# Optimization experiments

Measured on AMD Instinct MI355X. Metric: run time of the kernel, lower is better.

Reference implementation:

```python
import jax, jax.numpy as jnp
import numpy as np

DIM = 768
NUM_HEADS = 12
HEAD_DIM = DIM // NUM_HEADS
SCALE = HEAD_DIM ** -0.5


def setup_inputs() -> dict:
    key = jax.random.key(0)
    k1, k2, k3, k4 = jax.random.split(key, 4)
    x = jax.random.normal(k1, (8, 1024, DIM), dtype=jnp.float32)
    # torch Linear weights are [out, in]; no qkv bias (qkv_bias=False)
    qkv_w = jax.random.normal(k2, (3 * DIM, DIM), dtype=jnp.float32) * (DIM ** -0.5)
    proj_w = jax.random.normal(k3, (DIM, DIM), dtype=jnp.float32) * (DIM ** -0.5)
    proj_b = jax.random.normal(k4, (DIM,), dtype=jnp.float32) * 0.02
    return {"x": x, "qkv_w": qkv_w, "proj_w": proj_w, "proj_b": proj_b}


def reference(x, qkv_w, proj_w, proj_b):
    B, N, C = x.shape
    # qkv: [B, N, 3C] -> [3, B, H, N, D]
    qkv = jnp.einsum('bnc,oc->bno', x, qkv_w)
    qkv = qkv.reshape(B, N, 3, NUM_HEADS, HEAD_DIM).transpose(2, 0, 3, 1, 4)
    q, k, v = qkv[0], qkv[1], qkv[2]
    attn = jnp.einsum('bhnd,bhmd->bhnm', q, k) * SCALE
    attn = jax.nn.softmax(attn, axis=-1)
    out = jnp.einsum('bhnm,bhmd->bhnd', attn, v)  # [B, H, N, D]
    out = out.transpose(0, 2, 1, 3).reshape(B, N, C)
    out = jnp.einsum('bnc,oc->bno', out, proj_w) + proj_b
    return out
```

## Files before the change

### kernel.cpp

```cpp
#include <hip/hip_runtime.h>

typedef short bf16x8 __attribute__((ext_vector_type(8)));
typedef float f32x4 __attribute__((ext_vector_type(4)));
typedef float f32x16 __attribute__((ext_vector_type(16)));

#define AS1 __attribute__((address_space(1)))
#define AS3 __attribute__((address_space(3)))

__device__ __forceinline__ void gload16(const void* g, void* l) {
  __builtin_amdgcn_global_load_lds((const AS1 void*)g, (AS3 void*)l, 16, 0, 0);
}

__device__ __forceinline__ unsigned short f2bf(float f) {
  union { float f; unsigned u; } v; v.f = f;
  unsigned r = v.u + 0x7FFFu + ((v.u >> 16) & 1u);
  return (unsigned short)(r >> 16);
}

__device__ __forceinline__ unsigned cvtpk(float a, float b) {
  unsigned r;
  asm("v_cvt_pk_bf16_f32 %0, %1, %2" : "=v"(r) : "v"(a), "v"(b));
  return r;
}
__device__ __forceinline__ void plswap(unsigned& d, unsigned& s) {
  asm("v_permlane32_swap_b32 %0, %1" : "+v"(d), "+v"(s));
}


__global__ __launch_bounds__(256) void cast_all(
    const float* __restrict__ x, const float* __restrict__ w1, const float* __restrict__ w2,
    unsigned short* __restrict__ xb, unsigned short* __restrict__ w1b,
    unsigned short* __restrict__ w2b) {
  int i = blockIdx.x * blockDim.x + threadIdx.x;
  const float* in; unsigned short* out;
  if (i < 1572864) { in = x; out = xb; }
  else if (i < 2015232) { i -= 1572864; in = w1; out = w1b; }
  else { i -= 2015232; in = w2; out = w2b; }
  float4 v = reinterpret_cast<const float4*>(in)[i];
  ushort4 o; o.x = f2bf(v.x); o.y = f2bf(v.y); o.z = f2bf(v.z); o.w = f2bf(v.w);
  reinterpret_cast<ushort4*>(out)[i] = o;
}

template<int MODE>
__global__ __launch_bounds__(256) void gemm128(
    const unsigned short* __restrict__ A, const unsigned short* __restrict__ B,
    int K, int N,
    unsigned short* __restrict__ Qh, unsigned short* __restrict__ Kh,
    unsigned short* __restrict__ Vt,
    float* __restrict__ Cf, const float* __restrict__ bias) {
  constexpr int BM = (MODE == 0) ? 128 : 64;
  constexpr int MREP = BM / 32;
  constexpr int NX = (MODE == 0) ? 18 : 6;
  constexpr int CPX = (MODE == 0) ? 144 : 96;
  __shared__ unsigned short Ab[BM * 64];
  __shared__ unsigned short Bb[128 * 64];
  const int tid = threadIdx.x, lane = tid & 63, wave = tid >> 6;
  const int l15 = lane & 15, lhi = lane >> 4;
  const int bid = blockIdx.x;
  const int s = (bid & 7) * CPX + (bid >> 3);
  const int m0 = (s / NX) * BM, n0 = (s % NX) * 128;
  const int wr = wave >> 1, wc = wave & 1;

  f32x4 acc[MREP][4] = {};

  const int srow = tid >> 3;
  const int scol = (((tid & 7) * 16) ^ ((srow & 7) << 4)) >> 1;
  const unsigned short* aSrc = A + (size_t)(m0 + srow) * K + scol;
  const unsigned short* bSrc = B + (size_t)(n0 + srow) * K + scol;
  char* ldsA = (char*)Ab + wave * 1024;
  char* ldsB = (char*)Bb + wave * 1024;

  const int rswz = (l15 & 7) << 4;

  for (int k0 = 0; k0 < K; k0 += 64) {
    __syncthreads();
#pragma unroll
    for (int i = 0; i < BM / 32; ++i)
      gload16(aSrc + k0 + (size_t)32 * K * i, ldsA + i * 4096);
#pragma unroll
    for (int i = 0; i < 4; ++i)
      gload16(bSrc + k0 + (size_t)32 * K * i, ldsB + i * 4096);
    __syncthreads();
#pragma unroll
    for (int ks = 0; ks < 2; ++ks) {
      bf16x8 af[MREP], bfr[4];
#pragma unroll
      for (int mm = 0; mm < MREP; ++mm)
        af[mm] = *reinterpret_cast<const bf16x8*>(
            (char*)Ab + (wr * (BM / 2) + mm * 16 + l15) * 128 + ((ks * 64 + lhi * 16) ^ rswz));
#pragma unroll
      for (int nn = 0; nn < 4; ++nn)
        bfr[nn] = *reinterpret_cast<const bf16x8*>(
            (char*)Bb + (wc * 64 + nn * 16 + l15) * 128 + ((ks * 64 + lhi * 16) ^ rswz));
#pragma unroll
      for (int mm = 0; mm < MREP; ++mm)
#pragma unroll
        for (int nn = 0; nn < 4; ++nn)
          acc[mm][nn] = __builtin_amdgcn_mfma_f32_16x16x32_bf16(af[mm], bfr[nn], acc[mm][nn], 0, 0, 0);
    }
  }

  if (MODE == 0) {
    const int region = (n0 >= 1536) ? 2 : (n0 >= 768 ? 1 : 0);
    const float qs = (region == 0) ? 0.125f * 1.44269504088896340736f : 1.f;
#pragma unroll
    for (int mm = 0; mm < MREP; ++mm) {
      int gm = m0 + wr * (BM / 2) + mm * 16 + lhi * 4;
      int bb = gm >> 10, nb = gm & 1023;
#pragma unroll
      for (int nn = 0; nn < 4; ++nn) {
        int gn = n0 + wc * 64 + nn * 16 + l15 - region * 768;
        int d = gn & 63, hh = gn >> 6;
        if (region == 2) {
          ushort4 o;
          o.x = f2bf(acc[mm][nn][0]); o.y = f2bf(acc[mm][nn][1]);
          o.z = f2bf(acc[mm][nn][2]); o.w = f2bf(acc[mm][nn][3]);
          *reinterpret_cast<ushort4*>(&Vt[((size_t)(bb * 12 + hh) * 64 + d) * 1024 + nb]) = o;
        } else {
          unsigned short* dst =
              (region == 0 ? Qh : Kh) + ((size_t)(bb * 12 + hh) * 1024 + nb) * 64 + d;
#pragma unroll
          for (int r = 0; r < 4; ++r) dst[(size_t)r * 64] = f2bf(acc[mm][nn][r] * qs);
        }
      }
    }
  } else {
#pragma unroll
    for (int mm = 0; mm < MREP; ++mm) {
      int gm = m0 + wr * (BM / 2) + mm * 16 + lhi * 4;
#pragma unroll
      for (int nn = 0; nn < 4; ++nn) {
        int gn = n0 + wc * 64 + nn * 16 + l15;
        float bv = bias[gn];
#pragma unroll
        for (int r = 0; r < 4; ++r)
          Cf[(size_t)(gm + r) * N + gn] = acc[mm][nn][r] + bv;
      }
    }
  }
}

__global__ __launch_bounds__(256) void attn_kernel(
    const unsigned short* __restrict__ qh, const unsigned short* __restrict__ kh,
    const unsigned short* __restrict__ vt, unsigned short* __restrict__ aout) {
  __shared__ unsigned short KT[3][4096];
  __shared__ unsigned short VT[3][4096];

  const int tid = threadIdx.x, lane = tid & 63, wave = tid >> 6;
  const int l31 = lane & 31, hi = lane >> 5;
  const int bh = blockIdx.x % 96, qt = blockIdx.x / 96;
  const int b = bh / 12, h = bh % 12;

  const int srow = tid >> 3;
  const int scol = (((tid & 7) * 16) ^ ((srow & 7) << 4)) >> 1;
  const unsigned short* kS0 = kh + ((size_t)bh * 1024 + srow) * 64 + scol;
  const unsigned short* kS1 = kS0 + (size_t)32 * 64;
  const unsigned short* vS0 = vt + ((size_t)bh * 64 + srow) * 1024 + scol;
  const unsigned short* vS1 = vS0 + (size_t)32 * 1024;
  char* kDb = (char*)&KT[0][0] + wave * 1024;
  char* vDb = (char*)&VT[0][0] + wave * 1024;

  const int qw0 = qt * 128 + wave * 32;
  const unsigned short* qbase = qh + ((size_t)bh * 1024 + qw0 + l31) * 64 + hi * 8;
  bf16x8 qf[4];
#pragma unroll
  for (int ks = 0; ks < 4; ++ks)
    qf[ks] = *reinterpret_cast<const bf16x8*>(qbase + ks * 16);

  f32x16 oacc[2] = {};
  float lsum = 0.f;

  const int swz = (l31 & 7) << 4;
  const int rowb = l31 * 128;

  auto mkfrag = [&](const f32x16& e, int s8) -> bf16x8 {
    unsigned A0 = cvtpk(e[s8 + 0], e[s8 + 1]);
    unsigned A1 = cvtpk(e[s8 + 2], e[s8 + 3]);
    unsigned B0 = cvtpk(e[s8 + 4], e[s8 + 5]);
    unsigned B1 = cvtpk(e[s8 + 6], e[s8 + 7]);
    plswap(A0, B0);
    plswap(A1, B1);
    union { unsigned u[4]; bf16x8 v; } wu;
    wu.u[0] = A0; wu.u[1] = A1; wu.u[2] = B0; wu.u[3] = B1;
    return wu.v;
  };

  auto qkt = [&](const char* kb, f32x16& r0, f32x16& r1) {
    __builtin_amdgcn_s_setprio(1);
#pragma unroll
    for (int ks = 0; ks < 4; ++ks) {
      bf16x8 k0 = *reinterpret_cast<const bf16x8*>(kb + rowb + ((ks * 32 + hi * 16) ^ swz));
      bf16x8 k1 = *reinterpret_cast<const bf16x8*>(kb + 4096 + rowb + ((ks * 32 + hi * 16) ^ swz));
      r0 = __builtin_amdgcn_mfma_f32_32x32x16_bf16(k0, qf[ks], r0, 0, 0, 0);
      r1 = __builtin_amdgcn_mfma_f32_32x32x16_bf16(k1, qf[ks], r1, 0, 0, 0);
    }
    __builtin_amdgcn_s_setprio(0);
  };

#pragma unroll
  for (int t = 0; t < 2; ++t) {
    const int kv = t * 64;
    char* kd = kDb + t * 8192;
    char* vd = vDb + t * 8192;
    gload16(kS0 + (size_t)kv * 64, kd); gload16(kS1 + (size_t)kv * 64, kd + 4096);
    gload16(vS0 + kv, vd); gload16(vS1 + kv, vd + 4096);
  }
  asm volatile("s_waitcnt vmcnt(4)" ::: "memory");
  __builtin_amdgcn_s_barrier();
  f32x16 pn0 = {}, pn1 = {};
  qkt((const char*)&KT[0][0], pn0, pn1);

  for (int kt = 0; kt < 16; ++kt) {
    const int cur = kt % 3;
    asm volatile("s_waitcnt vmcnt(0)" ::: "memory");
    __builtin_amdgcn_s_barrier();
    if (kt + 2 <= 15) {
      const int kv = (kt + 2) * 64;
      const int nb = (kt + 2) % 3;
      char* kd = kDb + nb * 8192;
      char* vd = vDb + nb * 8192;
      gload16(kS0 + (size_t)kv * 64, kd); gload16(kS1 + (size_t)kv * 64, kd + 4096);
      gload16(vS0 + kv, vd); gload16(vS1 + kv, vd + 4096);
    }

    f32x16 p0 = pn0, p1 = pn1;
    if (kt < 15) {
      pn0 = f32x16{}; pn1 = f32x16{};
      qkt((const char*)&KT[(kt + 1) % 3][0], pn0, pn1);
    }

#pragma unroll
    for (int i = 0; i < 16; ++i) {
      p0[i] = __builtin_amdgcn_exp2f(p0[i]);
      p1[i] = __builtin_amdgcn_exp2f(p1[i]);
    }
    float su[8];
#pragma unroll
    for (int i = 0; i < 8; ++i)
      su[i] = (p0[i] + p0[i + 8]) + (p1[i] + p1[i + 8]);
    float s4[4];
#pragma unroll
    for (int i = 0; i < 4; ++i) s4[i] = su[i] + su[i + 4];
    lsum += (s4[0] + s4[1]) + (s4[2] + s4[3]);

    bf16x8 pb[4];
    pb[0] = mkfrag(p0, 0); pb[1] = mkfrag(p0, 8);
    pb[2] = mkfrag(p1, 0); pb[3] = mkfrag(p1, 8);

    const char* vb = (const char*)&VT[cur][0];
    __builtin_amdgcn_s_setprio(1);
#pragma unroll
    for (int kseg = 0; kseg < 4; ++kseg) {
      bf16x8 v0 = *reinterpret_cast<const bf16x8*>(vb + rowb + ((kseg * 32 + hi * 16) ^ swz));
      bf16x8 v1 = *reinterpret_cast<const bf16x8*>(vb + 4096 + rowb + ((kseg * 32 + hi * 16) ^ swz));
      oacc[0] = __builtin_amdgcn_mfma_f32_32x32x16_bf16(v0, pb[kseg], oacc[0], 0, 0, 0);
      oacc[1] = __builtin_amdgcn_mfma_f32_32x32x16_bf16(v1, pb[kseg], oacc[1], 0, 0, 0);
    }
    __builtin_amdgcn_s_setprio(0);
  }

  lsum += __shfl_xor(lsum, 32, 64);
  float inv = 1.f / lsum;
#pragma unroll
  for (int dblk = 0; dblk < 2; ++dblk)
#pragma unroll
    for (int g = 0; g < 4; ++g) {
      ushort4 o;
      o.x = f2bf(oacc[dblk][4 * g + 0] * inv);
      o.y = f2bf(oacc[dblk][4 * g + 1] * inv);
      o.z = f2bf(oacc[dblk][4 * g + 2] * inv);
      o.w = f2bf(oacc[dblk][4 * g + 3] * inv);
      int d = dblk * 32 + 8 * g + 4 * hi;
      *reinterpret_cast<ushort4*>(
          aout + ((size_t)(b * 1024 + qw0 + l31)) * 768 + h * 64 + d) = o;
    }
}

extern "C" void kernel_launch(void* const* d_in, const int* in_sizes, int n_in,
                              void* d_out, int out_size, void* d_ws, size_t ws_size,
                              hipStream_t stream) {
  const float* x      = (const float*)d_in[0];
  const float* qkv_w  = (const float*)d_in[1];
  const float* proj_w = (const float*)d_in[2];
  const float* proj_b = (const float*)d_in[3];
  float* out = (float*)d_out;

  char* ws = (char*)d_ws;
  unsigned short* xb     = (unsigned short*)(ws);
  unsigned short* wqkvb  = (unsigned short*)(ws + 12582912);
  unsigned short* wprojb = (unsigned short*)(ws + 16121856);
  unsigned short* qhb    = (unsigned short*)(ws + 17301504);
  unsigned short* khb    = (unsigned short*)(ws + 29884416);
  unsigned short* vtb    = (unsigned short*)(ws + 42467328);
  unsigned short* aob    = (unsigned short*)(ws + 55050240);

  cast_all<<<8448, 256, 0, stream>>>(x, qkv_w, proj_w, xb, wqkvb, wprojb);

  gemm128<0><<<1152, 256, 0, stream>>>(xb, wqkvb, 768, 2304, qhb, khb, vtb, nullptr, nullptr);

  attn_kernel<<<96 * 8, 256, 0, stream>>>(qhb, khb, vtb, aob);

  gemm128<1><<<768, 256, 0, stream>>>(aob, wprojb, 768, 768, nullptr, nullptr, nullptr, out, proj_b);
}
```

Before: 106.0 us.

## Double-buffer LDS tiles in GEMM to overlap global loads with MFMA

Splits the A/B shared-memory tiles into two buffers and prefetches the next k-tile with global_load_lds while MFMAs run on the current one. One vmcnt wait plus barrier per iteration replaces the two __syncthreads. The goal is to hide global-memory latency in the QKV and projection GEMMs. It doubles LDS usage per block, which may reduce occupancy.

```diff
diff --git a/kernel.cpp b/kernel.cpp
--- a/kernel.cpp
+++ b/kernel.cpp
@@ -52,8 +52,10 @@
   constexpr int MREP = BM / 32;
   constexpr int NX = (MODE == 0) ? 18 : 6;
   constexpr int CPX = (MODE == 0) ? 144 : 96;
-  __shared__ unsigned short Ab[BM * 64];
-  __shared__ unsigned short Bb[128 * 64];
+  constexpr int ABYTES = BM * 64 * 2;
+  constexpr int BBYTES = 128 * 64 * 2;
+  __shared__ unsigned short Ab[2][BM * 64];
+  __shared__ unsigned short Bb[2][128 * 64];
   const int tid = threadIdx.x, lane = tid & 63, wave = tid >> 6;
   const int l15 = lane & 15, lhi = lane >> 4;
   const int bid = blockIdx.x;
@@ -67,37 +69,51 @@
   const int scol = (((tid & 7) * 16) ^ ((srow & 7) << 4)) >> 1;
   const unsigned short* aSrc = A + (size_t)(m0 + srow) * K + scol;
   const unsigned short* bSrc = B + (size_t)(n0 + srow) * K + scol;
-  char* ldsA = (char*)Ab + wave * 1024;
-  char* ldsB = (char*)Bb + wave * 1024;
+  char* ldsA = (char*)&Ab[0][0] + wave * 1024;
+  char* ldsB = (char*)&Bb[0][0] + wave * 1024;
 
   const int rswz = (l15 & 7) << 4;
 
+  auto stage = [&](int buf, int k0) {
+#pragma unroll
+    for (int i = 0; i < BM / 32; ++i)
+      gload16(aSrc + k0 + (size_t)32 * K * i, ldsA + buf * ABYTES + i * 4096);
+#pragma unroll
+    for (int i = 0; i < 4; ++i)
+      gload16(bSrc + k0 + (size_t)32 * K * i, ldsB + buf * BBYTES + i * 4096);
+  };
+
+  stage(0, 0);
+  asm volatile("s_waitcnt vmcnt(0)" ::: "memory");
+  __builtin_amdgcn_s_barrier();
+
+  int cur = 0;
   for (int k0 = 0; k0 < K; k0 += 64) {
-    __syncthreads();
-#pragma unroll
-    for (int i = 0; i < BM / 32; ++i)
-      gload16(aSrc + k0 + (size_t)32 * K * i, ldsA + i * 4096);
-#pragma unroll
-    for (int i = 0; i < 4; ++i)
-      gload16(bSrc + k0 + (size_t)32 * K * i, ldsB + i * 4096);
-    __syncthreads();
+    if (k0 + 64 < K) stage(cur ^ 1, k0 + 64);
+
+    const char* abuf = (const char*)&Ab[0][0] + cur * ABYTES;
+    const char* bbuf = (const char*)&Bb[0][0] + cur * BBYTES;
 #pragma unroll
     for (int ks = 0; ks < 2; ++ks) {
       bf16x8 af[MREP], bfr[4];
 #pragma unroll
       for (int mm = 0; mm < MREP; ++mm)
         af[mm] = *reinterpret_cast<const bf16x8*>(
-            (char*)Ab + (wr * (BM / 2) + mm * 16 + l15) * 128 + ((ks * 64 + lhi * 16) ^ rswz));
+            abuf + (wr * (BM / 2) + mm * 16 + l15) * 128 + ((ks * 64 + lhi * 16) ^ rswz));
 #pragma unroll
       for (int nn = 0; nn < 4; ++nn)
         bfr[nn] = *reinterpret_cast<const bf16x8*>(
-            (char*)Bb + (wc * 64 + nn * 16 + l15) * 128 + ((ks * 64 + lhi * 16) ^ rswz));
+            bbuf + (wc * 64 + nn * 16 + l15) * 128 + ((ks * 64 + lhi * 16) ^ rswz));
 #pragma unroll
       for (int mm = 0; mm < MREP; ++mm)
 #pragma unroll
         for (int nn = 0; nn < 4; ++nn)
           acc[mm][nn] = __builtin_amdgcn_mfma_f32_16x16x32_bf16(af[mm], bfr[nn], acc[mm][nn], 0, 0, 0);
     }
+
+    asm volatile("s_waitcnt vmcnt(0)" ::: "memory");
+    __builtin_amdgcn_s_barrier();
+    cur ^= 1;
   }
 
   if (MODE == 0) {
```

New measurement: 113.6 us. 1.07x slower.

## Switch attention K/V staging from triple to double buffering with split K/V prefetch

Applied to the files above, without the earlier changes.

The attention kernel's K and V shared-memory staging drops from three buffers to two, cutting shared memory per block from 48KB to 32KB so more blocks can fit on a CU. To keep the two-buffer scheme safe, the prefetch of K tile kt+2 is issued right after the top barrier, since its buffer is no longer read. The prefetch of V tile kt+2 is issued after a new end-of-iteration barrier, once the PV MFMAs have finished reading that buffer. The wait counts are reworked so only the needed loads are waited on, at the price of an extra barrier per iteration and a shorter prefetch distance for V.

```diff
diff --git a/kernel.cpp b/kernel.cpp
--- a/kernel.cpp
+++ b/kernel.cpp
@@ -143,8 +143,8 @@
 __global__ __launch_bounds__(256) void attn_kernel(
     const unsigned short* __restrict__ qh, const unsigned short* __restrict__ kh,
     const unsigned short* __restrict__ vt, unsigned short* __restrict__ aout) {
-  __shared__ unsigned short KT[3][4096];
-  __shared__ unsigned short VT[3][4096];
+  __shared__ unsigned short KT[2][4096];
+  __shared__ unsigned short VT[2][4096];
 
   const int tid = threadIdx.x, lane = tid & 63, wave = tid >> 6;
   const int l31 = lane & 31, hi = lane >> 5;
@@ -159,6 +159,19 @@
   const unsigned short* vS1 = vS0 + (size_t)32 * 1024;
   char* kDb = (char*)&KT[0][0] + wave * 1024;
   char* vDb = (char*)&VT[0][0] + wave * 1024;
+
+  auto stageK = [&](int kt2, int buf) {
+    const int kv = kt2 * 64;
+    char* kd = kDb + buf * 8192;
+    gload16(kS0 + (size_t)kv * 64, kd);
+    gload16(kS1 + (size_t)kv * 64, kd + 4096);
+  };
+  auto stageV = [&](int kt2, int buf) {
+    const int kv = kt2 * 64;
+    char* vd = vDb + buf * 8192;
+    gload16(vS0 + kv, vd);
+    gload16(vS1 + kv, vd + 4096);
+  };
 
   const int qw0 = qt * 128 + wave * 32;
   const unsigned short* qbase = qh + ((size_t)bh * 1024 + qw0 + l31) * 64 + hi * 8;
@@ -197,36 +210,28 @@
     __builtin_amdgcn_s_setprio(0);
   };
 
-#pragma unroll
-  for (int t = 0; t < 2; ++t) {
-    const int kv = t * 64;
-    char* kd = kDb + t * 8192;
-    char* vd = vDb + t * 8192;
-    gload16(kS0 + (size_t)kv * 64, kd); gload16(kS1 + (size_t)kv * 64, kd + 4096);
-    gload16(vS0 + kv, vd); gload16(vS1 + kv, vd + 4096);
-  }
-  asm volatile("s_waitcnt vmcnt(4)" ::: "memory");
+  stageK(0, 0); stageV(0, 0);
+  stageK(1, 1); stageV(1, 1);
+  asm volatile("s_waitcnt vmcnt(6)" ::: "memory");
   __builtin_amdgcn_s_barrier();
   f32x16 pn0 = {}, pn1 = {};
   qkt((const char*)&KT[0][0], pn0, pn1);
 
   for (int kt = 0; kt < 16; ++kt) {
-    const int cur = kt % 3;
-    asm volatile("s_waitcnt vmcnt(0)" ::: "memory");
+    const int cur = kt & 1;
+    if (kt < 15) {
+      asm volatile("s_waitcnt vmcnt(2)" ::: "memory");
+    } else {
+      asm volatile("s_waitcnt vmcnt(0)" ::: "memory");
+    }
     __builtin_amdgcn_s_barrier();
-    if (kt + 2 <= 15) {
-      const int kv = (kt + 2) * 64;
-      const int nb = (kt + 2) % 3;
-      char* kd = kDb + nb * 8192;
-      char* vd = vDb + nb * 8192;
-      gload16(kS0 + (size_t)kv * 64, kd); gload16(kS1 + (size_t)kv * 64, kd + 4096);
-      gload16(vS0 + kv, vd); gload16(vS1 + kv, vd + 4096);
-    }
+
+    if (kt + 2 <= 15) stageK(kt + 2, cur);
 
     f32x16 p0 = pn0, p1 = pn1;
     if (kt < 15) {
       pn0 = f32x16{}; pn1 = f32x16{};
-      qkt((const char*)&KT[(kt + 1) % 3][0], pn0, pn1);
+      qkt((const char*)&KT[(kt + 1) & 1][0], pn0, pn1);
     }
 
 #pragma unroll
@@ -257,6 +262,9 @@
       oacc[1] = __builtin_amdgcn_mfma_f32_32x32x16_bf16(v1, pb[kseg], oacc[1], 0, 0, 0);
     }
     __builtin_amdgcn_s_setprio(0);
+
+    __builtin_amdgcn_s_barrier();
+    if (kt + 2 <= 15) stageV(kt + 2, cur);
   }
 
   lsum += __shfl_xor(lsum, 32, 64);
```

Result: no change. 105.5 us, median of 2 (-0.5%).
